# Optimization experiments

Measured on AMD Instinct MI355X. Metric: run time of the kernel, lower is better.

Reference implementation:

```python
import jax, jax.numpy as jnp
import numpy as np

N_NODES = 50000
N_EDGES = 600000
D = 128


def setup_inputs() -> dict:
    key = jax.random.key(0)
    k1, k2, k3, k4, k5, k6 = jax.random.split(key, 6)
    x = jax.random.normal(k1, (N_NODES, D), dtype=jnp.float32)
    edge_index = jax.random.randint(k2, (2, N_EDGES), 0, N_NODES, dtype=jnp.int64)
    # nn.Linear default init: U(-1/sqrt(fan_in), 1/sqrt(fan_in))
    bound = 1.0 / np.sqrt(D)
    W1 = jax.random.uniform(k3, (D, D), minval=-bound, maxval=bound, dtype=jnp.float32)
    b1 = jax.random.uniform(k4, (D,), minval=-bound, maxval=bound, dtype=jnp.float32)
    W2 = jax.random.uniform(k5, (D, D), minval=-bound, maxval=bound, dtype=jnp.float32)
    b2 = jax.random.uniform(k6, (D,), minval=-bound, maxval=bound, dtype=jnp.float32)
    return {"x": x, "edge_index": edge_index, "W1": W1, "b1": b1, "W2": W2, "b2": b2}


def reference(x, edge_index, W1, b1, W2, b2):
    row, col = edge_index[0], edge_index[1]
    n = x.shape[0]
    # degree of each node as aggregation target, clamped to >= 1
    deg = jax.ops.segment_sum(jnp.ones(row.shape, dtype=x.dtype), row, num_segments=n)
    deg = jnp.maximum(deg, 1.0)[:, None]  # [N, 1]
    # round 1: gather neighbors, scatter-add by row, normalize, linear+relu
    agg = jax.ops.segment_sum(x[col], row, num_segments=n)  # [N, D]
    h = jax.nn.relu((agg / deg) @ W1.T + b1)
    # round 2
    agg2 = jax.ops.segment_sum(h[col], row, num_segments=n)  # [N, D]
    return jax.nn.relu((agg2 / deg) @ W2.T + b2)
```

## Files before the change

kernel.cpp:

```cpp
#include <hip/hip_runtime.h>
#include <hip/hip_fp16.h>

#define D 128
#define TILE_R 64

typedef _Float16 h8 __attribute__((ext_vector_type(8)));
typedef float f4 __attribute__((ext_vector_type(4)));

__global__ __launch_bounds__(256) void prep_kernel(int* __restrict__ hist, int n,
                                                   const float* __restrict__ W1,
                                                   __half* __restrict__ WB1,
                                                   const float* __restrict__ W2,
                                                   __half* __restrict__ WB2) {
    if (blockIdx.x < 2) {
        const float* W = blockIdx.x ? W2 : W1;
        __half* WB     = blockIdx.x ? WB2 : WB1;
        for (int idx = threadIdx.x; idx < D * D; idx += 256) {
            int j  = idx & 7;
            int l  = (idx >> 3) & 63;
            int kk = (idx >> 9) & 3;
            int c  = idx >> 11;
            int k   = kk * 32 + (l >> 4) * 8 + j;
            int col = c * 16 + (l & 15);
            WB[idx] = __float2half(W[col * D + k]);
        }
        return;
    }
    int i = (blockIdx.x - 2) * 256 + threadIdx.x;
    if (i < n) hist[i] = 0;
}

__device__ inline h8 load_frag(const __half* p) { return *(const h8*)p; }
__device__ inline h8 load_frag(const float* p) {
    float4 u = *(const float4*)p;
    float4 v = *(const float4*)(p + 4);
    h8 r;
    r[0] = (_Float16)u.x; r[1] = (_Float16)u.y; r[2] = (_Float16)u.z; r[3] = (_Float16)u.w;
    r[4] = (_Float16)v.x; r[5] = (_Float16)v.y; r[6] = (_Float16)v.z; r[7] = (_Float16)v.w;
    return r;
}

template <typename T>
__device__ inline void linear_coal(const T* __restrict__ src,
                                   const __half* __restrict__ WB,
                                   __half* __restrict__ z, int n, int blk) {
    __shared__ __half Zs[64][132];
    int l    = threadIdx.x & 63;
    int wv   = threadIdx.x >> 6;
    int row0 = blk * TILE_R + wv * 16;
    int arow = row0 + (l & 15);
    bool rowok = arow < n;

    h8 a[4];
#pragma unroll
    for (int kk = 0; kk < 4; ++kk) {
        if (rowok)
            a[kk] = load_frag(&src[(size_t)arow * D + kk * 32 + (l >> 4) * 8]);
        else
            a[kk] = (h8)(_Float16)0.0f;
    }

    int lr0 = wv * 16 + (l >> 4) * 4;
#pragma unroll
    for (int c = 0; c < 8; ++c) {
        f4 acc = {0.f, 0.f, 0.f, 0.f};
#pragma unroll
        for (int kk = 0; kk < 4; ++kk) {
            h8 b = *(const h8*)&WB[(((c * 4 + kk) * 64) + l) * 8];
            acc = __builtin_amdgcn_mfma_f32_16x16x32_f16(a[kk], b, acc, 0, 0, 0);
        }
        int col = c * 16 + (l & 15);
#pragma unroll
        for (int r = 0; r < 4; ++r) Zs[lr0 + r][col] = __float2half(acc[r]);
    }
    __syncthreads();

    int row = threadIdx.x >> 2;
    int cb  = (threadIdx.x & 3) * 32;
    int gro = blk * TILE_R + row;
    if (gro < n) {
        float2 p0 = *(const float2*)&Zs[row][cb];
        float2 p1 = *(const float2*)&Zs[row][cb + 4];
        float2 p2 = *(const float2*)&Zs[row][cb + 8];
        float2 p3 = *(const float2*)&Zs[row][cb + 12];
        float2 p4 = *(const float2*)&Zs[row][cb + 16];
        float2 p5 = *(const float2*)&Zs[row][cb + 20];
        float2 p6 = *(const float2*)&Zs[row][cb + 24];
        float2 p7 = *(const float2*)&Zs[row][cb + 28];
        __half* zp = &z[(size_t)gro * D + cb];
        *(float4*)(zp)      = make_float4(p0.x, p0.y, p1.x, p1.y);
        *(float4*)(zp + 8)  = make_float4(p2.x, p2.y, p3.x, p3.y);
        *(float4*)(zp + 16) = make_float4(p4.x, p4.y, p5.x, p5.y);
        *(float4*)(zp + 24) = make_float4(p6.x, p6.y, p7.x, p7.y);
    }
}

__global__ __launch_bounds__(256) void hist_linear_kernel(const int* __restrict__ ei, int e,
                                                          int* __restrict__ hist, int nhist,
                                                          const float* __restrict__ x,
                                                          const __half* __restrict__ WB,
                                                          __half* __restrict__ z, int n) {
    if (blockIdx.x < nhist) {
        int i = blockIdx.x * 256 + threadIdx.x;
        if (i < e) atomicAdd(&hist[ei[i]], 1);
        return;
    }
    linear_coal<float>(x, WB, z, n, blockIdx.x - nhist);
}

__global__ __launch_bounds__(256) void partial_kernel(const int* __restrict__ hist,
                                                      int* __restrict__ bsum, int n) {
    int i = blockIdx.x * 256 + threadIdx.x;
    int v = (i < n) ? hist[i] : 0;
#pragma unroll
    for (int off = 1; off < 64; off <<= 1) v += __shfl_xor(v, off);
    __shared__ int ws[4];
    int lane = threadIdx.x & 63, w = threadIdx.x >> 6;
    if (lane == 0) ws[w] = v;
    __syncthreads();
    if (threadIdx.x == 0) bsum[blockIdx.x] = ws[0] + ws[1] + ws[2] + ws[3];
}

__global__ __launch_bounds__(256) void finalize_kernel(const int* __restrict__ hist,
                                                       const int* __restrict__ bsum,
                                                       int* __restrict__ offsets,
                                                       int* __restrict__ cursor,
                                                       float* __restrict__ rdeg, int n) {
    __shared__ int wt[4];
    int t = threadIdx.x, lane = t & 63, w = t >> 6;

    int p = 0;
    for (int k = t; k < blockIdx.x; k += 256) p += bsum[k];
#pragma unroll
    for (int off = 1; off < 64; off <<= 1) p += __shfl_xor(p, off);
    if (lane == 0) wt[w] = p;
    __syncthreads();
    int blockbase = wt[0] + wt[1] + wt[2] + wt[3];
    __syncthreads();

    int i = blockIdx.x * 256 + t;
    int v = (i < n) ? hist[i] : 0;
    int iv = v;
#pragma unroll
    for (int off = 1; off < 64; off <<= 1) {
        int n2 = __shfl_up(iv, off);
        if (lane >= off) iv += n2;
    }
    if (lane == 63) wt[w] = iv;
    __syncthreads();
    int add = blockbase;
    for (int k = 0; k < w; ++k) add += wt[k];
    int excl = iv - v + add;
    if (i < n) {
        offsets[i] = excl;
        cursor[i]  = excl;
        rdeg[i]    = 1.0f / fmaxf((float)v, 1.0f);
    }
}

__global__ __launch_bounds__(256) void fill_kernel(const int* __restrict__ ei, int e,
                                                   int* __restrict__ cursor,
                                                   int* __restrict__ csr) {
    int i = blockIdx.x * blockDim.x + threadIdx.x;
    if (i < e) {
        int r = ei[i];
        int c = ei[e + i];
        int pos = atomicAdd(&cursor[r], 1);
        csr[pos] = c;
    }
}

__device__ inline void addh8(float* a, float4 v) {
    const __half2* h = (const __half2*)&v;
    float2 f0 = __half22float2(h[0]);
    float2 f1 = __half22float2(h[1]);
    float2 f2 = __half22float2(h[2]);
    float2 f3 = __half22float2(h[3]);
    a[0] += f0.x; a[1] += f0.y; a[2] += f1.x; a[3] += f1.y;
    a[4] += f2.x; a[5] += f2.y; a[6] += f3.x; a[7] += f3.y;
}

__device__ inline void gather_core(const float4* __restrict__ base, int start, int cnt,
                                   int gl, const int* __restrict__ csr, float* acc) {
    int i = 0;
    for (; i + 8 <= cnt; i += 8) {
        int c0 = csr[start + i];
        int c1 = csr[start + i + 1];
        int c2 = csr[start + i + 2];
        int c3 = csr[start + i + 3];
        int c4 = csr[start + i + 4];
        int c5 = csr[start + i + 5];
        int c6 = csr[start + i + 6];
        int c7 = csr[start + i + 7];
        float4 v0 = base[(size_t)c0 * 16 + gl];
        float4 v1 = base[(size_t)c1 * 16 + gl];
        float4 v2 = base[(size_t)c2 * 16 + gl];
        float4 v3 = base[(size_t)c3 * 16 + gl];
        float4 v4 = base[(size_t)c4 * 16 + gl];
        float4 v5 = base[(size_t)c5 * 16 + gl];
        float4 v6 = base[(size_t)c6 * 16 + gl];
        float4 v7 = base[(size_t)c7 * 16 + gl];
        addh8(acc, v0); addh8(acc, v1); addh8(acc, v2); addh8(acc, v3);
        addh8(acc, v4); addh8(acc, v5); addh8(acc, v6); addh8(acc, v7);
    }
    if (i + 4 <= cnt) {
        int c0 = csr[start + i];
        int c1 = csr[start + i + 1];
        int c2 = csr[start + i + 2];
        int c3 = csr[start + i + 3];
        float4 v0 = base[(size_t)c0 * 16 + gl];
        float4 v1 = base[(size_t)c1 * 16 + gl];
        float4 v2 = base[(size_t)c2 * 16 + gl];
        float4 v3 = base[(size_t)c3 * 16 + gl];
        addh8(acc, v0); addh8(acc, v1); addh8(acc, v2); addh8(acc, v3);
        i += 4;
    }
    int rem = cnt - i;
    if (rem > 0) {
        int c0 = csr[start + i];
        int c1 = csr[start + min(i + 1, cnt - 1)];
        int c2 = csr[start + min(i + 2, cnt - 1)];
        float4 v0 = base[(size_t)c0 * 16 + gl];
        float4 v1 = base[(size_t)c1 * 16 + gl];
        float4 v2 = base[(size_t)c2 * 16 + gl];
        addh8(acc, v0);
        if (rem > 1) addh8(acc, v1);
        if (rem > 2) addh8(acc, v2);
    }
}

__global__ __launch_bounds__(512) void gather_linear_kernel(const __half* __restrict__ z1,
                                                            const int* __restrict__ offsets,
                                                            const int* __restrict__ hist,
                                                            const int* __restrict__ csr,
                                                            const float* __restrict__ rdeg,
                                                            const float* __restrict__ bias,
                                                            const __half* __restrict__ WB2,
                                                            __half* __restrict__ z2, int n) {
    __shared__ __half Hs[32][136];
    int t    = threadIdx.x;
    int wv   = t >> 6;
    int lane = t & 63;
    int g    = lane >> 4;
    int gl   = lane & 15;
    int lrow = wv * 4 + g;
    int node = blockIdx.x * 32 + lrow;

    if (node < n) {
        float acc[8] = {0.f, 0.f, 0.f, 0.f, 0.f, 0.f, 0.f, 0.f};
        gather_core((const float4*)z1, offsets[node], hist[node], gl, csr, acc);
        float rd = rdeg[node];
        float4 b0 = ((const float4*)bias)[gl * 2];
        float4 b1 = ((const float4*)bias)[gl * 2 + 1];
        __half2 hp[4];
        hp[0] = __float22half2_rn(make_float2(fmaxf(acc[0] * rd + b0.x, 0.f),
                                              fmaxf(acc[1] * rd + b0.y, 0.f)));
        hp[1] = __float22half2_rn(make_float2(fmaxf(acc[2] * rd + b0.z, 0.f),
                                              fmaxf(acc[3] * rd + b0.w, 0.f)));
        hp[2] = __float22half2_rn(make_float2(fmaxf(acc[4] * rd + b1.x, 0.f),
                                              fmaxf(acc[5] * rd + b1.y, 0.f)));
        hp[3] = __float22half2_rn(make_float2(fmaxf(acc[6] * rd + b1.z, 0.f),
                                              fmaxf(acc[7] * rd + b1.w, 0.f)));
        *(float4*)&Hs[lrow][gl * 8] = *(const float4*)hp;
    }
    __syncthreads();

    int r0 = (wv >> 2) * 16;
    int arow = r0 + (lane & 15);
    h8 a[4];
#pragma unroll
    for (int kk = 0; kk < 4; ++kk)
        a[kk] = *(const h8*)&Hs[arow][kk * 32 + (lane >> 4) * 8];

    int srow = blockIdx.x * 32 + r0 + (lane >> 4) * 4;
#pragma unroll
    for (int cc = 0; cc < 2; ++cc) {
        int c = (wv & 3) * 2 + cc;
        f4 acc = {0.f, 0.f, 0.f, 0.f};
#pragma unroll
        for (int kk = 0; kk < 4; ++kk) {
            h8 b = *(const h8*)&WB2[(((c * 4 + kk) * 64) + lane) * 8];
            acc = __builtin_amdgcn_mfma_f32_16x16x32_f16(a[kk], b, acc, 0, 0, 0);
        }
        int col = c * 16 + (lane & 15);
#pragma unroll
        for (int r = 0; r < 4; ++r) {
            int ro = srow + r;
            if (ro < n) z2[(size_t)ro * D + col] = __float2half(acc[r]);
        }
    }
}

__global__ __launch_bounds__(256) void gather_kernel(const __half* __restrict__ z,
                                                     const int* __restrict__ offsets,
                                                     const int* __restrict__ hist,
                                                     const int* __restrict__ csr,
                                                     const float* __restrict__ rdeg,
                                                     const float* __restrict__ bias,
                                                     float* __restrict__ out, int n) {
    int tid  = blockIdx.x * 256 + threadIdx.x;
    int wave = tid >> 6;
    int lane = threadIdx.x & 63;
    int g    = lane >> 4;
    int gl   = lane & 15;
    int node = wave * 4 + g;
    if (node >= n) return;

    float acc[8] = {0.f, 0.f, 0.f, 0.f, 0.f, 0.f, 0.f, 0.f};
    gather_core((const float4*)z, offsets[node], hist[node], gl, csr, acc);

    float rd = rdeg[node];
    float4 b0 = ((const float4*)bias)[gl * 2];
    float4 b1 = ((const float4*)bias)[gl * 2 + 1];
    float4* o4 = (float4*)out;
    o4[(size_t)node * 32 + gl * 2] =
        make_float4(fmaxf(acc[0] * rd + b0.x, 0.f), fmaxf(acc[1] * rd + b0.y, 0.f),
                    fmaxf(acc[2] * rd + b0.z, 0.f), fmaxf(acc[3] * rd + b0.w, 0.f));
    o4[(size_t)node * 32 + gl * 2 + 1] =
        make_float4(fmaxf(acc[4] * rd + b1.x, 0.f), fmaxf(acc[5] * rd + b1.y, 0.f),
                    fmaxf(acc[6] * rd + b1.z, 0.f), fmaxf(acc[7] * rd + b1.w, 0.f));
}

extern "C" void kernel_launch(void* const* d_in, const int* in_sizes, int n_in,
                              void* d_out, int out_size, void* d_ws, size_t ws_size,
                              hipStream_t stream) {
    const float* x  = (const float*)d_in[0];
    const int*   ei = (const int*)d_in[1];
    const float* W1 = (const float*)d_in[2];
    const float* b1 = (const float*)d_in[3];
    const float* W2 = (const float*)d_in[4];
    const float* b2 = (const float*)d_in[5];
    float* out = (float*)d_out;

    int N = in_sizes[0] / D;
    int E = in_sizes[1] / 2;
    int NB = (N + 255) / 256;

    int* hist    = (int*)d_ws;
    int* offsets = hist + N;
    int* cursor  = offsets + N;
    int* csr     = cursor + N;
    float* rdeg  = (float*)(csr + E);
    int* bsum    = (int*)(rdeg + N);
    __half* WB1  = (__half*)(bsum + ((NB + 3) & ~3));
    __half* WB2  = WB1 + D * D;
    __half* zz   = WB2 + D * D;
    __half* zz2  = zz + (size_t)N * D;

    int nhist = (E + 255) / 256;
    int nblk  = (N + TILE_R - 1) / TILE_R;
    int gfblk = (N + 31) / 32;
    int gblk  = ((N + 3) / 4 * 64 + 255) / 256;

    prep_kernel<<<NB + 2, 256, 0, stream>>>(hist, N, W1, WB1, W2, WB2);
    hist_linear_kernel<<<nhist + nblk, 256, 0, stream>>>(ei, E, hist, nhist, x, WB1, zz, N);
    partial_kernel<<<NB, 256, 0, stream>>>(hist, bsum, N);
    finalize_kernel<<<NB, 256, 0, stream>>>(hist, bsum, offsets, cursor, rdeg, N);
    fill_kernel<<<(E + 255) / 256, 256, 0, stream>>>(ei, E, cursor, csr);
    gather_linear_kernel<<<gfblk, 512, 0, stream>>>(zz, offsets, hist, csr, rdeg, b1,
                                                    WB2, zz2, N);
    gather_kernel<<<gblk, 256, 0, stream>>>(zz2, offsets, hist, csr, rdeg, b2, out, N);
}
```

Measured before the change: 161.5 us.

## Privatize degree histogram and fill cursors into eight per-chunk copies

The degree histogram and the CSR fill cursors are split into eight private copies, selected by block index modulo 8, so that atomics on the same node are spread over separate addresses. The finalize step sums the copies and gives each copy its own sub-range starting offset, and the node degree is stored in a separate array. The hist blocks are also moved after the linear blocks in the combined launch. This adds zeroing and reading of eight times more counter memory. The privatization also requires the histogram pass and the fill pass to map edges to chunks identically.

```diff
diff --git a/kernel.cpp b/kernel.cpp
--- a/kernel.cpp
+++ b/kernel.cpp
@@ -3,11 +3,12 @@
 
 #define D 128
 #define TILE_R 64
+#define NC 8
 
 typedef _Float16 h8 __attribute__((ext_vector_type(8)));
 typedef float f4 __attribute__((ext_vector_type(4)));
 
-__global__ __launch_bounds__(256) void prep_kernel(int* __restrict__ hist, int n,
+__global__ __launch_bounds__(256) void prep_kernel(int* __restrict__ hist8, int n8,
                                                    const float* __restrict__ W1,
                                                    __half* __restrict__ WB1,
                                                    const float* __restrict__ W2,
@@ -27,7 +28,7 @@
         return;
     }
     int i = (blockIdx.x - 2) * 256 + threadIdx.x;
-    if (i < n) hist[i] = 0;
+    if (i < n8) hist8[i] = 0;
 }
 
 __device__ inline h8 load_frag(const __half* p) { return *(const h8*)p; }
@@ -96,22 +97,27 @@
 }
 
 __global__ __launch_bounds__(256) void hist_linear_kernel(const int* __restrict__ ei, int e,
-                                                          int* __restrict__ hist, int nhist,
+                                                          int* __restrict__ hist8, int nlin,
                                                           const float* __restrict__ x,
                                                           const __half* __restrict__ WB,
                                                           __half* __restrict__ z, int n) {
-    if (blockIdx.x < nhist) {
-        int i = blockIdx.x * 256 + threadIdx.x;
-        if (i < e) atomicAdd(&hist[ei[i]], 1);
+    if (blockIdx.x >= nlin) {
+        int chunk = blockIdx.x - nlin;
+        int i = chunk * 256 + threadIdx.x;
+        if (i < e) atomicAdd(&hist8[(chunk & (NC - 1)) * n + ei[i]], 1);
         return;
     }
-    linear_coal<float>(x, WB, z, n, blockIdx.x - nhist);
-}
-
-__global__ __launch_bounds__(256) void partial_kernel(const int* __restrict__ hist,
+    linear_coal<float>(x, WB, z, n, blockIdx.x);
+}
+
+__global__ __launch_bounds__(256) void partial_kernel(const int* __restrict__ hist8,
                                                       int* __restrict__ bsum, int n) {
     int i = blockIdx.x * 256 + threadIdx.x;
-    int v = (i < n) ? hist[i] : 0;
+    int v = 0;
+    if (i < n) {
+#pragma unroll
+        for (int c = 0; c < NC; ++c) v += hist8[c * n + i];
+    }
 #pragma unroll
     for (int off = 1; off < 64; off <<= 1) v += __shfl_xor(v, off);
     __shared__ int ws[4];
@@ -121,10 +127,11 @@
     if (threadIdx.x == 0) bsum[blockIdx.x] = ws[0] + ws[1] + ws[2] + ws[3];
 }
 
-__global__ __launch_bounds__(256) void finalize_kernel(const int* __restrict__ hist,
+__global__ __launch_bounds__(256) void finalize_kernel(const int* __restrict__ hist8,
                                                        const int* __restrict__ bsum,
                                                        int* __restrict__ offsets,
-                                                       int* __restrict__ cursor,
+                                                       int* __restrict__ deg,
+                                                       int* __restrict__ cursor8,
                                                        float* __restrict__ rdeg, int n) {
     __shared__ int wt[4];
     int t = threadIdx.x, lane = t & 63, w = t >> 6;
@@ -139,8 +146,16 @@
     __syncthreads();
 
     int i = blockIdx.x * 256 + t;
-    int v = (i < n) ? hist[i] : 0;
-    int iv = v;
+    int cnt[NC];
+    int tot = 0;
+    if (i < n) {
+#pragma unroll
+        for (int c = 0; c < NC; ++c) { cnt[c] = hist8[c * n + i]; tot += cnt[c]; }
+    } else {
+#pragma unroll
+        for (int c = 0; c < NC; ++c) cnt[c] = 0;
+    }
+    int iv = tot;
 #pragma unroll
     for (int off = 1; off < 64; off <<= 1) {
         int n2 = __shfl_up(iv, off);
@@ -150,22 +165,25 @@
     __syncthreads();
     int add = blockbase;
     for (int k = 0; k < w; ++k) add += wt[k];
-    int excl = iv - v + add;
+    int excl = iv - tot + add;
     if (i < n) {
         offsets[i] = excl;
-        cursor[i]  = excl;
-        rdeg[i]    = 1.0f / fmaxf((float)v, 1.0f);
+        deg[i]     = tot;
+        rdeg[i]    = 1.0f / fmaxf((float)tot, 1.0f);
+        int run = excl;
+#pragma unroll
+        for (int c = 0; c < NC; ++c) { cursor8[c * n + i] = run; run += cnt[c]; }
     }
 }
 
 __global__ __launch_bounds__(256) void fill_kernel(const int* __restrict__ ei, int e,
-                                                   int* __restrict__ cursor,
-                                                   int* __restrict__ csr) {
-    int i = blockIdx.x * blockDim.x + threadIdx.x;
+                                                   int* __restrict__ cursor8,
+                                                   int* __restrict__ csr, int n) {
+    int i = blockIdx.x * 256 + threadIdx.x;
     if (i < e) {
         int r = ei[i];
         int c = ei[e + i];
-        int pos = atomicAdd(&cursor[r], 1);
+        int pos = atomicAdd(&cursor8[(blockIdx.x & (NC - 1)) * n + r], 1);
         csr[pos] = c;
     }
 }
@@ -231,7 +249,7 @@
 
 __global__ __launch_bounds__(512) void gather_linear_kernel(const __half* __restrict__ z1,
                                                             const int* __restrict__ offsets,
-                                                            const int* __restrict__ hist,
+                                                            const int* __restrict__ deg,
                                                             const int* __restrict__ csr,
                                                             const float* __restrict__ rdeg,
                                                             const float* __restrict__ bias,
@@ -248,7 +266,7 @@
 
     if (node < n) {
         float acc[8] = {0.f, 0.f, 0.f, 0.f, 0.f, 0.f, 0.f, 0.f};
-        gather_core((const float4*)z1, offsets[node], hist[node], gl, csr, acc);
+        gather_core((const float4*)z1, offsets[node], deg[node], gl, csr, acc);
         float rd = rdeg[node];
         float4 b0 = ((const float4*)bias)[gl * 2];
         float4 b1 = ((const float4*)bias)[gl * 2 + 1];
@@ -293,7 +311,7 @@
 
 __global__ __launch_bounds__(256) void gather_kernel(const __half* __restrict__ z,
                                                      const int* __restrict__ offsets,
-                                                     const int* __restrict__ hist,
+                                                     const int* __restrict__ deg,
                                                      const int* __restrict__ csr,
                                                      const float* __restrict__ rdeg,
                                                      const float* __restrict__ bias,
@@ -307,7 +325,7 @@
     if (node >= n) return;
 
     float acc[8] = {0.f, 0.f, 0.f, 0.f, 0.f, 0.f, 0.f, 0.f};
-    gather_core((const float4*)z, offsets[node], hist[node], gl, csr, acc);
+    gather_core((const float4*)z, offsets[node], deg[node], gl, csr, acc);
 
     float rd = rdeg[node];
     float4 b0 = ((const float4*)bias)[gl * 2];
@@ -336,10 +354,11 @@
     int E = in_sizes[1] / 2;
     int NB = (N + 255) / 256;
 
-    int* hist    = (int*)d_ws;
-    int* offsets = hist + N;
-    int* cursor  = offsets + N;
-    int* csr     = cursor + N;
+    int* hist8   = (int*)d_ws;
+    int* cursor8 = hist8 + NC * N;
+    int* offsets = cursor8 + NC * N;
+    int* deg     = offsets + N;
+    int* csr     = deg + N;
     float* rdeg  = (float*)(csr + E);
     int* bsum    = (int*)(rdeg + N);
     __half* WB1  = (__half*)(bsum + ((NB + 3) & ~3));
@@ -347,17 +366,18 @@
     __half* zz   = WB2 + D * D;
     __half* zz2  = zz + (size_t)N * D;
 
+    int NB8   = (NC * N + 255) / 256;
     int nhist = (E + 255) / 256;
     int nblk  = (N + TILE_R - 1) / TILE_R;
     int gfblk = (N + 31) / 32;
     int gblk  = ((N + 3) / 4 * 64 + 255) / 256;
 
-    prep_kernel<<<NB + 2, 256, 0, stream>>>(hist, N, W1, WB1, W2, WB2);
-    hist_linear_kernel<<<nhist + nblk, 256, 0, stream>>>(ei, E, hist, nhist, x, WB1, zz, N);
-    partial_kernel<<<NB, 256, 0, stream>>>(hist, bsum, N);
-    finalize_kernel<<<NB, 256, 0, stream>>>(hist, bsum, offsets, cursor, rdeg, N);
-    fill_kernel<<<(E + 255) / 256, 256, 0, stream>>>(ei, E, cursor, csr);
-    gather_linear_kernel<<<gfblk, 512, 0, stream>>>(zz, offsets, hist, csr, rdeg, b1,
+    prep_kernel<<<NB8 + 2, 256, 0, stream>>>(hist8, NC * N, W1, WB1, W2, WB2);
+    hist_linear_kernel<<<nblk + nhist, 256, 0, stream>>>(ei, E, hist8, nblk, x, WB1, zz, N);
+    partial_kernel<<<NB, 256, 0, stream>>>(hist8, bsum, N);
+    finalize_kernel<<<NB, 256, 0, stream>>>(hist8, bsum, offsets, deg, cursor8, rdeg, N);
+    fill_kernel<<<nhist, 256, 0, stream>>>(ei, E, cursor8, csr, N);
+    gather_linear_kernel<<<gfblk, 512, 0, stream>>>(zz, offsets, deg, csr, rdeg, b1,
                                                     WB2, zz2, N);
-    gather_kernel<<<gblk, 256, 0, stream>>>(zz2, offsets, hist, csr, rdeg, b2, out, N);
-}
+    gather_kernel<<<gblk, 256, 0, stream>>>(zz2, offsets, deg, csr, rdeg, b2, out, N);
+}
```

Result: faster. 146.4 us (-9.4%).
